# Kernel tuning notes

Measured on AMD Instinct MI355X. Metric: run time of the kernel, lower is better.

Reference implementation:

```python
import jax, jax.numpy as jnp
import numpy as np

EMBED_DIM = 512
NUM_JOINTS = 17
HIDDEN = EMBED_DIM * 2  # hidden_ratio=2
B, T = 32, 243


def setup_inputs() -> dict:
    key = jax.random.key(0)
    k_x, k_w1, k_w2 = jax.random.split(key, 3)
    x = jax.random.normal(k_x, (B, T, NUM_JOINTS, EMBED_DIM), dtype=jnp.float32)
    # kaiming_uniform with a=sqrt(5): bound = sqrt(6 / ((1 + a^2) * fan_in)) = sqrt(1/fan_in)
    b1 = float(np.sqrt(1.0 / EMBED_DIM))
    fc1_w = jax.random.uniform(k_w1, (NUM_JOINTS, EMBED_DIM, HIDDEN), minval=-b1, maxval=b1, dtype=jnp.float32)
    fc1_b = jnp.zeros((NUM_JOINTS, HIDDEN), dtype=jnp.float32)
    b2 = float(np.sqrt(1.0 / HIDDEN))
    fc2_w = jax.random.uniform(k_w2, (NUM_JOINTS, HIDDEN, 3), minval=-b2, maxval=b2, dtype=jnp.float32)
    fc2_b = jnp.zeros((NUM_JOINTS, 3), dtype=jnp.float32)
    ln_gamma = jnp.ones((EMBED_DIM,), dtype=jnp.float32)
    ln_beta = jnp.zeros((EMBED_DIM,), dtype=jnp.float32)
    return {"x": x, "ln_gamma": ln_gamma, "ln_beta": ln_beta,
            "fc1_w": fc1_w, "fc1_b": fc1_b, "fc2_w": fc2_w, "fc2_b": fc2_b}


def _layernorm(x, gamma, beta, eps=1e-5):
    mu = jnp.mean(x, axis=-1, keepdims=True)
    var = jnp.mean(jnp.square(x - mu), axis=-1, keepdims=True)
    return (x - mu) * jax.lax.rsqrt(var + eps) * gamma + beta


def reference(x, ln_gamma, ln_beta, fc1_w, fc1_b, fc2_w, fc2_b):
    # x: [B, T, J, d] -> [B, T, J, 3]
    xn = _layernorm(x, ln_gamma, ln_beta)
    h = jnp.einsum('btjd,jdh->btjh', xn, fc1_w) + fc1_b  # [B,T,J,H]
    h = jax.nn.gelu(h, approximate=False)  # torch GELU default is exact (erf)
    y = jnp.einsum('btjh,jho->btjo', h, fc2_w) + fc2_b  # [B,T,J,3]
    return y
```

## Files before the change

kernel.cpp:

```cpp
#include <hip/hip_runtime.h>
#include <hip/hip_bf16.h>

#define JN   17
#define DIM  512
#define HID  1024
#define MTOT 7776
#define MPAD 7808
#define BN   256
#define NTHR 512

typedef __attribute__((ext_vector_type(8))) short s16x8;
typedef __attribute__((ext_vector_type(4))) float f32x4;
typedef unsigned short ushort_t;

__device__ __forceinline__ unsigned int f2bf(float f) {
    return (unsigned int)__builtin_bit_cast(unsigned short, __float2bfloat16(f));
}

__device__ __forceinline__ float gelu_erf(float h) {
    float ah = fabsf(h);
    float z  = ah * 0.7071067811865476f;
    float t  = __builtin_amdgcn_rcpf(fmaf(0.3275911f, z, 1.0f));
    float p  = fmaf(fmaf(fmaf(fmaf(1.061405429f, t, -1.453152027f), t,
                              1.421413741f), t, -0.284496736f), t, 0.254829592f);
    float er = 1.0f - p * t * __expf(-z * z);
    return fmaf(0.5f * ah, er, 0.5f * h);
}

__global__ __launch_bounds__(256)
void prep_w1(const float* __restrict__ w1, ushort_t* __restrict__ w1s) {
    int b  = blockIdx.x;
    int nq = b & 3;
    int kc = (b >> 2) & 15;
    int j  = b >> 6;
    int n  = nq * 256 + threadIdx.x;

    const float* src = w1 + ((size_t)j * DIM + kc * 32) * HID + n;
    ushort_t* dst = w1s + (((size_t)j * 16 + kc) * 1024 + n) * 32;

    #pragma unroll
    for (int u = 0; u < 4; ++u) {
        float v[8];
        #pragma unroll
        for (int e = 0; e < 8; ++e) v[e] = src[(u * 8 + e) * HID];
        uint4 qq;
        qq.x = f2bf(v[0]) | (f2bf(v[1]) << 16);
        qq.y = f2bf(v[2]) | (f2bf(v[3]) << 16);
        qq.z = f2bf(v[4]) | (f2bf(v[5]) << 16);
        qq.w = f2bf(v[6]) | (f2bf(v[7]) << 16);
        int p = u ^ ((n >> 1) & 3);
        *(uint4*)(dst + p * 8) = qq;
    }
}

__global__ __launch_bounds__(NTHR)
void prep_xn(const float* __restrict__ x,
             const float* __restrict__ gamma,
             const float* __restrict__ beta,
             ushort_t* __restrict__ xa)
{
    const int lane = threadIdx.x & 63;
    const int wv   = threadIdx.x >> 6;
    const int m    = blockIdx.x * 8 + wv;
    const int j    = blockIdx.y;

    const float4* gp = (const float4*)(gamma + lane * 8);
    const float4* bp = (const float4*)(beta + lane * 8);
    float4 g0 = gp[0], g1 = gp[1];
    float4 e0 = bp[0], e1 = bp[1];

    const float4* xp = (const float4*)(x + ((size_t)m * JN + j) * DIM + lane * 8);
    float4 va = xp[0], vb = xp[1];

    float s  = ((va.x + va.y) + (va.z + va.w)) + ((vb.x + vb.y) + (vb.z + vb.w));
    float s2 = fmaf(va.x, va.x, fmaf(va.y, va.y, fmaf(va.z, va.z, fmaf(va.w, va.w,
               fmaf(vb.x, vb.x, fmaf(vb.y, vb.y, fmaf(vb.z, vb.z, vb.w * vb.w)))))));
    #pragma unroll
    for (int d = 1; d < 64; d <<= 1) {
        s  += __shfl_xor(s,  d);
        s2 += __shfl_xor(s2, d);
    }
    float mu  = s * (1.0f / 512.0f);
    float var = s2 * (1.0f / 512.0f) - mu * mu;
    float rs  = rsqrtf(var + 1e-5f);

    float v0 = fmaf((va.x - mu) * rs, g0.x, e0.x);
    float v1 = fmaf((va.y - mu) * rs, g0.y, e0.y);
    float v2 = fmaf((va.z - mu) * rs, g0.z, e0.z);
    float v3 = fmaf((va.w - mu) * rs, g0.w, e0.w);
    float v4 = fmaf((vb.x - mu) * rs, g1.x, e1.x);
    float v5 = fmaf((vb.y - mu) * rs, g1.y, e1.y);
    float v6 = fmaf((vb.z - mu) * rs, g1.z, e1.z);
    float v7 = fmaf((vb.w - mu) * rs, g1.w, e1.w);
    uint4 qq;
    qq.x = f2bf(v0) | (f2bf(v1) << 16);
    qq.y = f2bf(v2) | (f2bf(v3) << 16);
    qq.z = f2bf(v4) | (f2bf(v5) << 16);
    qq.w = f2bf(v6) | (f2bf(v7) << 16);

    int kc = lane >> 2;
    int p  = (lane & 3) ^ (m & 3) ^ ((m >> 2) & 3);
    *(uint4*)(xa + (((size_t)j * 16 + kc) * MPAD + m) * 32 + p * 8) = qq;
}

#define SLOT6   24576
#define SMEM_V8 49152
#define NWG    (61 * 4 * JN)

__global__ __launch_bounds__(NTHR, 4)
void pjh_gemm_v8(const ushort_t* __restrict__ xa,
                 const ushort_t* __restrict__ w1s,
                 const float* __restrict__ b1,
                 const float* __restrict__ w2,
                 float* __restrict__ ypart)
{
    extern __shared__ char smem[];
    const int tid  = threadIdx.x;
    const int lane = tid & 63;
    const int wv   = tid >> 6;
    const int wm   = wv >> 2;
    const int wn   = wv & 3;

    const int q   = NWG / 8, r = NWG % 8;
    const int xcd = blockIdx.x & 7;
    const int lid = blockIdx.x >> 3;
    const int work = ((xcd < r) ? xcd * (q + 1) : r * (q + 1) + (xcd - r) * q) + lid;
    const int nt = work & 3;
    const int wrest = work >> 2;
    const int mt = wrest % 61;
    const int j  = wrest / 61;

    const ushort_t* aSrc = xa  + (size_t)j * 16 * MPAD * 32
                               + (size_t)mt * 128 * 32 + tid * 8;
    const ushort_t* bSrc = w1s + (size_t)j * 16 * 1024 * 32
                               + (size_t)nt * 256 * 32 + (size_t)(wv * 2) * 512 + lane * 8;

    int aoffs[4], boffs[4];
    {
        const int g = lane >> 4;
        #pragma unroll
        for (int mf = 0; mf < 4; ++mf) {
            int ml = wm * 64 + mf * 16 + (lane & 15);
            int p  = g ^ (ml & 3) ^ ((ml >> 2) & 3);
            aoffs[mf] = ml * 64 + p * 16;
        }
        #pragma unroll
        for (int nf = 0; nf < 4; ++nf) {
            int nl = wn * 64 + nf * 16 + (lane & 15);
            int p  = g ^ ((nl >> 1) & 3);
            boffs[nf] = 8192 + (nl * 4 + p) * 16;
        }
    }

#define ISSUE8(SBASE) do {                                                     \
        __builtin_amdgcn_global_load_lds(                                      \
            (const __attribute__((address_space(1))) unsigned int*)aSrc,       \
            (__attribute__((address_space(3))) unsigned int*)(smem + (SBASE) + wv * 1024), \
            16, 0, 0);                                                         \
        __builtin_amdgcn_global_load_lds(                                      \
            (const __attribute__((address_space(1))) unsigned int*)bSrc,       \
            (__attribute__((address_space(3))) unsigned int*)(smem + (SBASE) + 8192 + wv * 2048), \
            16, 0, 0);                                                         \
        __builtin_amdgcn_global_load_lds(                                      \
            (const __attribute__((address_space(1))) unsigned int*)(bSrc + 512), \
            (__attribute__((address_space(3))) unsigned int*)(smem + (SBASE) + 8192 + wv * 2048 + 1024), \
            16, 0, 0);                                                         \
        aSrc += (size_t)MPAD * 32;                                             \
        bSrc += 32768;                                                         \
    } while (0)

#define STEP8(SBASE) do {                                                      \
        s16x8 aF[4], bF[4];                                                    \
        _Pragma("unroll")                                                      \
        for (int mf = 0; mf < 4; ++mf)                                         \
            aF[mf] = *(const s16x8*)(smem + (SBASE) + aoffs[mf]);              \
        _Pragma("unroll")                                                      \
        for (int nf = 0; nf < 4; ++nf)                                         \
            bF[nf] = *(const s16x8*)(smem + (SBASE) + boffs[nf]);              \
        __builtin_amdgcn_s_setprio(1);                                         \
        _Pragma("unroll")                                                      \
        for (int mf = 0; mf < 4; ++mf)                                         \
            _Pragma("unroll")                                                  \
            for (int nf = 0; nf < 4; ++nf)                                     \
                acc[mf][nf] = __builtin_amdgcn_mfma_f32_16x16x32_bf16(aF[mf], bF[nf], acc[mf][nf], 0, 0, 0); \
        __builtin_amdgcn_s_setprio(0);                                         \
    } while (0)

    const f32x4 zero4 = {0.f, 0.f, 0.f, 0.f};
    f32x4 acc[4][4];
    #pragma unroll
    for (int mf = 0; mf < 4; ++mf)
        #pragma unroll
        for (int nf = 0; nf < 4; ++nf) acc[mf][nf] = zero4;

    ISSUE8(0);
    __syncthreads();

    #pragma unroll 1
    for (int tp = 0; tp < 8; ++tp) {
        ISSUE8(SLOT6);
        STEP8(0);
        __syncthreads();
        if (tp < 7) {
            ISSUE8(0);
        }
        STEP8(SLOT6);
        __syncthreads();
    }

    float yr[4][4][3];
    #pragma unroll
    for (int a = 0; a < 4; ++a)
        #pragma unroll
        for (int rr = 0; rr < 4; ++rr)
            #pragma unroll
            for (int o = 0; o < 3; ++o) yr[a][rr][o] = 0.f;

    #pragma unroll
    for (int nf = 0; nf < 4; ++nf) {
        int n = nt * BN + wn * 64 + nf * 16 + (lane & 15);
        float b1v = b1[j * HID + n];
        const float* w2p = w2 + ((size_t)j * HID + n) * 3;
        float w20 = w2p[0], w21 = w2p[1], w22 = w2p[2];
        #pragma unroll
        for (int mf = 0; mf < 4; ++mf) {
            #pragma unroll
            for (int rr = 0; rr < 4; ++rr) {
                float gv = gelu_erf(acc[mf][nf][rr] + b1v);
                yr[mf][rr][0] = fmaf(gv, w20, yr[mf][rr][0]);
                yr[mf][rr][1] = fmaf(gv, w21, yr[mf][rr][1]);
                yr[mf][rr][2] = fmaf(gv, w22, yr[mf][rr][2]);
            }
        }
    }

    #pragma unroll
    for (int mf = 0; mf < 4; ++mf)
        #pragma unroll
        for (int rr = 0; rr < 4; ++rr)
            #pragma unroll
            for (int o = 0; o < 3; ++o) {
                float v = yr[mf][rr][o];
                v += __shfl_xor(v, 1);
                v += __shfl_xor(v, 2);
                v += __shfl_xor(v, 4);
                v += __shfl_xor(v, 8);
                yr[mf][rr][o] = v;
            }

    float* Yp = (float*)smem;
    if ((lane & 15) == 0) {
        int mrow = lane >> 4;
        #pragma unroll
        for (int mf = 0; mf < 4; ++mf)
            #pragma unroll
            for (int rr = 0; rr < 4; ++rr) {
                int m = wm * 64 + mf * 16 + mrow * 4 + rr;
                #pragma unroll
                for (int o = 0; o < 3; ++o)
                    Yp[(wn * 128 + m) * 3 + o] = yr[mf][rr][o];
            }
    }
    __syncthreads();

    if (tid < 128 * 3) {
        int m = tid / 3;
        int o = tid - m * 3;
        int gr = mt * 128 + m;
        float v = Yp[m * 3 + o] + Yp[(128 + m) * 3 + o]
                + Yp[(2 * 128 + m) * 3 + o] + Yp[(3 * 128 + m) * 3 + o];
        ypart[(((size_t)nt * MPAD + gr) * JN + j) * 3 + o] = v;
    }
#undef ISSUE8
#undef STEP8
}

__global__ __launch_bounds__(512)
void fc2_reduce(const float* __restrict__ ypart,
                const float* __restrict__ b2,
                float* __restrict__ out)
{
    int idx = blockIdx.x * 512 + threadIdx.x;
    if (idx >= MTOT * JN * 3) return;
    int rest = idx / 3;
    int o = idx - rest * 3;
    int j = rest % JN;
    float v = b2[j * 3 + o]
            + ypart[idx]
            + ypart[(size_t)MPAD * JN * 3 + idx]
            + ypart[(size_t)2 * MPAD * JN * 3 + idx]
            + ypart[(size_t)3 * MPAD * JN * 3 + idx];
    out[idx] = v;
}

#define BM3 96
#define A3_OFF 0
#define B3_OFF 98304
#define Y3_OFF 98304
#define SMEM_V3 163840

__global__ __launch_bounds__(NTHR, 2)
void pjh_fused_v3(const float* __restrict__ x,
                  const float* __restrict__ gamma,
                  const float* __restrict__ beta,
                  const ushort_t* __restrict__ w1s,
                  const float* __restrict__ b1,
                  const float* __restrict__ w2,
                  const float* __restrict__ b2,
                  float* __restrict__ out)
{
    extern __shared__ char smem[];
    const int tid  = threadIdx.x;
    const int lane = tid & 63;
    const int wv   = tid >> 6;
    const int wm   = wv >> 2;
    const int wn   = wv & 3;
    const int mt   = blockIdx.x;
    const int j    = blockIdx.y;

    const ushort_t* w1j = w1s + (size_t)j * 16 * 1024 * 32;

    #pragma unroll
    for (int tt = 0; tt < 2; ++tt) {
        const ushort_t* tb = w1j + (size_t)tt * 1024 * 32;
        #pragma unroll
        for (int qq = 0; qq < 2; ++qq) {
            const ushort_t* src = tb + (size_t)(wv * 2 + qq) * 512 + lane * 8;
            void* dst = smem + B3_OFF + tt * 16384 + (wv * 2 + qq) * 1024;
            __builtin_amdgcn_global_load_lds(
                (const __attribute__((address_space(1))) unsigned int*)src,
                (__attribute__((address_space(3))) unsigned int*)dst, 16, 0, 0);
        }
    }

    {
        const float4* gp  = (const float4*)(gamma + lane * 8);
        const float4* bpp = (const float4*)(beta + lane * 8);
        float4 g0 = gp[0], g1 = gp[1];
        float4 e0 = bpp[0], e1 = bpp[1];
        #pragma unroll
        for (int rb = 0; rb < 12; rb += 4) {
            float4 xs[4][2];
            #pragma unroll
            for (int rr = 0; rr < 4; ++rr) {
                int gr = mt * BM3 + wv * 12 + rb + rr;
                const float4* xp = (const float4*)(x + ((size_t)gr * JN + j) * DIM + lane * 8);
                xs[rr][0] = xp[0]; xs[rr][1] = xp[1];
            }
            #pragma unroll
            for (int rr = 0; rr < 4; ++rr) {
                int m = wv * 12 + rb + rr;
                float4 va = xs[rr][0], vb = xs[rr][1];
                float s  = ((va.x + va.y) + (va.z + va.w)) + ((vb.x + vb.y) + (vb.z + vb.w));
                float s2 = fmaf(va.x, va.x, fmaf(va.y, va.y, fmaf(va.z, va.z, fmaf(va.w, va.w,
                           fmaf(vb.x, vb.x, fmaf(vb.y, vb.y, fmaf(vb.z, vb.z, vb.w * vb.w)))))));
                #pragma unroll
                for (int d = 1; d < 64; d <<= 1) {
                    s  += __shfl_xor(s,  d);
                    s2 += __shfl_xor(s2, d);
                }
                float mu  = s * (1.0f / 512.0f);
                float var = s2 * (1.0f / 512.0f) - mu * mu;
                float rs  = rsqrtf(var + 1e-5f);
                float v0 = fmaf((va.x - mu) * rs, g0.x, e0.x);
                float v1 = fmaf((va.y - mu) * rs, g0.y, e0.y);
                float v2 = fmaf((va.z - mu) * rs, g0.z, e0.z);
                float v3 = fmaf((va.w - mu) * rs, g0.w, e0.w);
                float v4 = fmaf((vb.x - mu) * rs, g1.x, e1.x);
                float v5 = fmaf((vb.y - mu) * rs, g1.y, e1.y);
                float v6 = fmaf((vb.z - mu) * rs, g1.z, e1.z);
                float v7 = fmaf((vb.w - mu) * rs, g1.w, e1.w);
                uint4 qq;
                qq.x = f2bf(v0) | (f2bf(v1) << 16);
                qq.y = f2bf(v2) | (f2bf(v3) << 16);
                qq.z = f2bf(v4) | (f2bf(v5) << 16);
                qq.w = f2bf(v6) | (f2bf(v7) << 16);
                *(uint4*)(smem + A3_OFF + m * 1024 + ((lane ^ (m & 7)) * 16)) = qq;
            }
        }
    }

    __syncthreads();

    float yr[3][4][3];
    #pragma unroll
    for (int a = 0; a < 3; ++a)
        #pragma unroll
        for (int rr = 0; rr < 4; ++rr)
            #pragma unroll
            for (int o = 0; o < 3; ++o) yr[a][rr][o] = 0.f;

    const f32x4 zero4 = {0.f, 0.f, 0.f, 0.f};
    f32x4 acc[3][4];
    #pragma unroll
    for (int mf = 0; mf < 3; ++mf)
        #pragma unroll
        for (int nf = 0; nf < 4; ++nf) acc[mf][nf] = zero4;

    #pragma unroll 1
    for (int t = 0; t < 64; ++t) {
        if (t + 2 < 64) {
            int kc = (t + 2) & 15, nt = (t + 2) >> 4;
            const ushort_t* tb = w1j + ((size_t)kc * 1024 + nt * 256) * 32;
            int bb = ((t + 2) & 3) * 16384;
            #pragma unroll
            for (int qq = 0; qq < 2; ++qq) {
                const ushort_t* src = tb + (size_t)(wv * 2 + qq) * 512 + lane * 8;
                void* dst = smem + B3_OFF + bb + (wv * 2 + qq) * 1024;
                __builtin_amdgcn_global_load_lds(
                    (const __attribute__((address_space(1))) unsigned int*)src,
                    (__attribute__((address_space(3))) unsigned int*)dst, 16, 0, 0);
            }
        }

        int kc = t & 15;
        int bb = (t & 3) * 16384;
        int g  = lane >> 4;
        s16x8 aF[3], bF[4];
        #pragma unroll
        for (int mf = 0; mf < 3; ++mf) {
            int m  = wm * 48 + mf * 16 + (lane & 15);
            int ul = kc * 4 + g;
            aF[mf] = *(const s16x8*)(smem + A3_OFF + m * 1024 + ((ul ^ (m & 7)) * 16));
        }
        #pragma unroll
        for (int nf = 0; nf < 4; ++nf) {
            int nl = wn * 64 + nf * 16 + (lane & 15);
            int p  = g ^ ((nl >> 1) & 3);
            bF[nf] = *(const s16x8*)(smem + B3_OFF + bb + (nl * 4 + p) * 16);
        }

        __builtin_amdgcn_s_setprio(1);
        #pragma unroll
        for (int mf = 0; mf < 3; ++mf)
            #pragma unroll
            for (int nf = 0; nf < 4; ++nf)
                acc[mf][nf] = __builtin_amdgcn_mfma_f32_16x16x32_bf16(aF[mf], bF[nf], acc[mf][nf], 0, 0, 0);
        __builtin_amdgcn_s_setprio(0);

        if ((t & 15) == 15) {
            int nt = t >> 4;
            #pragma unroll
            for (int nf = 0; nf < 4; ++nf) {
                int n = nt * BN + wn * 64 + nf * 16 + (lane & 15);
                float b1v = b1[j * HID + n];
                const float* w2p = w2 + ((size_t)j * HID + n) * 3;
                float w20 = w2p[0], w21 = w2p[1], w22 = w2p[2];
                #pragma unroll
                for (int mf = 0; mf < 3; ++mf) {
                    #pragma unroll
                    for (int rr = 0; rr < 4; ++rr) {
                        float gv = gelu_erf(acc[mf][nf][rr] + b1v);
                        yr[mf][rr][0] = fmaf(gv, w20, yr[mf][rr][0]);
                        yr[mf][rr][1] = fmaf(gv, w21, yr[mf][rr][1]);
                        yr[mf][rr][2] = fmaf(gv, w22, yr[mf][rr][2]);
                    }
                }
            }
            #pragma unroll
            for (int mf = 0; mf < 3; ++mf)
                #pragma unroll
                for (int nf = 0; nf < 4; ++nf)
                    acc[mf][nf] = zero4;
        }

        if (t < 62) {
            asm volatile("s_waitcnt vmcnt(2)" ::: "memory");
        } else {
            asm volatile("s_waitcnt vmcnt(0)" ::: "memory");
        }
        __builtin_amdgcn_s_barrier();
    }

    #pragma unroll
    for (int mf = 0; mf < 3; ++mf)
        #pragma unroll
        for (int rr = 0; rr < 4; ++rr)
            #pragma unroll
            for (int o = 0; o < 3; ++o) {
                float v = yr[mf][rr][o];
                v += __shfl_xor(v, 1);
                v += __shfl_xor(v, 2);
                v += __shfl_xor(v, 4);
                v += __shfl_xor(v, 8);
                yr[mf][rr][o] = v;
            }

    __syncthreads();

    float* Yp = (float*)(smem + Y3_OFF);
    if ((lane & 15) == 0) {
        int mrow = lane >> 4;
        #pragma unroll
        for (int mf = 0; mf < 3; ++mf)
            #pragma unroll
            for (int rr = 0; rr < 4; ++rr) {
                int m = wm * 48 + mf * 16 + mrow * 4 + rr;
                #pragma unroll
                for (int o = 0; o < 3; ++o)
                    Yp[(wn * BM3 + m) * 3 + o] = yr[mf][rr][o];
            }
    }
    __syncthreads();

    if (tid < BM3 * 3) {
        int m = tid / 3;
        int o = tid - m * 3;
        int gr = mt * BM3 + m;
        float v = Yp[m * 3 + o] + Yp[(BM3 + m) * 3 + o]
                + Yp[(2 * BM3 + m) * 3 + o] + Yp[(3 * BM3 + m) * 3 + o]
                + b2[j * 3 + o];
        out[((size_t)gr * JN + j) * 3 + o] = v;
    }
}

extern "C" void kernel_launch(void* const* d_in, const int* in_sizes, int n_in,
                              void* d_out, int out_size, void* d_ws, size_t ws_size,
                              hipStream_t stream) {
    (void)in_sizes; (void)n_in; (void)out_size;
    const float* x   = (const float*)d_in[0];
    const float* ga  = (const float*)d_in[1];
    const float* be  = (const float*)d_in[2];
    const float* w1  = (const float*)d_in[3];
    const float* b1  = (const float*)d_in[4];
    const float* w2  = (const float*)d_in[5];
    const float* b2  = (const float*)d_in[6];
    float* out = (float*)d_out;

    const size_t xa_bytes  = (size_t)JN * 16 * MPAD * 32 * sizeof(ushort_t);
    const size_t w1s_bytes = (size_t)JN * 16 * 1024 * 32 * sizeof(ushort_t);
    const size_t yp_bytes  = (size_t)4 * MPAD * JN * 3 * sizeof(float);

    if (ws_size >= xa_bytes + w1s_bytes + yp_bytes) {
        ushort_t* xa  = (ushort_t*)d_ws;
        ushort_t* w1s = (ushort_t*)((char*)d_ws + xa_bytes);
        float* ypart  = (float*)((char*)d_ws + xa_bytes + w1s_bytes);
        prep_xn<<<dim3(MTOT / 8, JN), NTHR, 0, stream>>>(x, ga, be, xa);
        prep_w1<<<JN * 16 * 4, 256, 0, stream>>>(w1, w1s);
        hipFuncSetAttribute((const void*)pjh_gemm_v8,
                            hipFuncAttributeMaxDynamicSharedMemorySize, SMEM_V8);
        pjh_gemm_v8<<<NWG, NTHR, SMEM_V8, stream>>>(xa, w1s, b1, w2, ypart);
        fc2_reduce<<<(MTOT * JN * 3 + 511) / 512, 512, 0, stream>>>(ypart, b2, out);
    } else {
        ushort_t* w1s = (ushort_t*)d_ws;
        prep_w1<<<JN * 16 * 4, 256, 0, stream>>>(w1, w1s);
        hipFuncSetAttribute((const void*)pjh_fused_v3,
                            hipFuncAttributeMaxDynamicSharedMemorySize, SMEM_V3);
        dim3 grid(MTOT / BM3, JN);
        pjh_fused_v3<<<grid, NTHR, SMEM_V3, stream>>>(x, ga, be, w1s, b1, w2, b2, out);
    }
}
```

Measured before the change: 315.7 us.

## Load MFMA fragments directly from global into registers, dropping LDS staging

The GEMM kernel no longer stages A and B tiles through LDS with global_load_lds and barriers. Each wave now loads its bf16 fragments straight from global memory into a double-buffered register set. The tile shrinks to 128x128 with 256 threads, so the N dimension splits into 8 partial outputs and the reduction kernel sums 8 slices. The xa layout drops its swizzle to match the direct loads. This removes LDS traffic and synchronisation, at the cost of redundant global/L2 reads across waves, higher register pressure and a larger partial-sum buffer.

```diff
diff --git a/kernel.cpp b/kernel.cpp
--- a/kernel.cpp
+++ b/kernel.cpp
@@ -6,7 +6,6 @@
 #define HID  1024
 #define MTOT 7776
 #define MPAD 7808
-#define BN   256
 #define NTHR 512
 
 typedef __attribute__((ext_vector_type(8))) short s16x8;
@@ -99,90 +98,56 @@
     qq.w = f2bf(v6) | (f2bf(v7) << 16);
 
     int kc = lane >> 2;
-    int p  = (lane & 3) ^ (m & 3) ^ ((m >> 2) & 3);
-    *(uint4*)(xa + (((size_t)j * 16 + kc) * MPAD + m) * 32 + p * 8) = qq;
-}
-
-#define SLOT6   24576
-#define SMEM_V8 49152
-#define NWG    (61 * 4 * JN)
-
-__global__ __launch_bounds__(NTHR, 4)
-void pjh_gemm_v8(const ushort_t* __restrict__ xa,
+    *(uint4*)(xa + (((size_t)j * 16 + kc) * MPAD + m) * 32 + (lane & 3) * 8) = qq;
+}
+
+#define NWG9 (61 * 8 * JN)
+
+__global__ __launch_bounds__(256, 3)
+void pjh_gemm_v9(const ushort_t* __restrict__ xa,
                  const ushort_t* __restrict__ w1s,
                  const float* __restrict__ b1,
                  const float* __restrict__ w2,
                  float* __restrict__ ypart)
 {
-    extern __shared__ char smem[];
+    __shared__ float Yp[2 * 128 * 3];
     const int tid  = threadIdx.x;
     const int lane = tid & 63;
     const int wv   = tid >> 6;
-    const int wm   = wv >> 2;
-    const int wn   = wv & 3;
-
-    const int q   = NWG / 8, r = NWG % 8;
-    const int xcd = blockIdx.x & 7;
-    const int lid = blockIdx.x >> 3;
-    const int work = ((xcd < r) ? xcd * (q + 1) : r * (q + 1) + (xcd - r) * q) + lid;
-    const int nt = work & 3;
-    const int wrest = work >> 2;
-    const int mt = wrest % 61;
-    const int j  = wrest / 61;
-
-    const ushort_t* aSrc = xa  + (size_t)j * 16 * MPAD * 32
-                               + (size_t)mt * 128 * 32 + tid * 8;
-    const ushort_t* bSrc = w1s + (size_t)j * 16 * 1024 * 32
-                               + (size_t)nt * 256 * 32 + (size_t)(wv * 2) * 512 + lane * 8;
-
-    int aoffs[4], boffs[4];
-    {
-        const int g = lane >> 4;
-        #pragma unroll
-        for (int mf = 0; mf < 4; ++mf) {
-            int ml = wm * 64 + mf * 16 + (lane & 15);
-            int p  = g ^ (ml & 3) ^ ((ml >> 2) & 3);
-            aoffs[mf] = ml * 64 + p * 16;
-        }
-        #pragma unroll
-        for (int nf = 0; nf < 4; ++nf) {
-            int nl = wn * 64 + nf * 16 + (lane & 15);
-            int p  = g ^ ((nl >> 1) & 3);
-            boffs[nf] = 8192 + (nl * 4 + p) * 16;
-        }
-    }
-
-#define ISSUE8(SBASE) do {                                                     \
-        __builtin_amdgcn_global_load_lds(                                      \
-            (const __attribute__((address_space(1))) unsigned int*)aSrc,       \
-            (__attribute__((address_space(3))) unsigned int*)(smem + (SBASE) + wv * 1024), \
-            16, 0, 0);                                                         \
-        __builtin_amdgcn_global_load_lds(                                      \
-            (const __attribute__((address_space(1))) unsigned int*)bSrc,       \
-            (__attribute__((address_space(3))) unsigned int*)(smem + (SBASE) + 8192 + wv * 2048), \
-            16, 0, 0);                                                         \
-        __builtin_amdgcn_global_load_lds(                                      \
-            (const __attribute__((address_space(1))) unsigned int*)(bSrc + 512), \
-            (__attribute__((address_space(3))) unsigned int*)(smem + (SBASE) + 8192 + wv * 2048 + 1024), \
-            16, 0, 0);                                                         \
-        aSrc += (size_t)MPAD * 32;                                             \
-        bSrc += 32768;                                                         \
+    const int wm   = wv >> 1;
+    const int wn   = wv & 1;
+
+    const int xcd  = blockIdx.x & 7;
+    const int lid  = blockIdx.x >> 3;
+    const int work = xcd * (NWG9 / 8) + lid;
+    const int nt2  = work & 7;
+    const int wrest = work >> 3;
+    const int mt   = wrest % 61;
+    const int j    = wrest / 61;
+
+    const int g = lane >> 4;
+    const ushort_t* aB = xa + (size_t)j * 16 * MPAD * 32
+                            + ((size_t)mt * 128 + wm * 64 + (lane & 15)) * 32 + g * 8;
+    const int pB = g ^ (((lane & 15) >> 1) & 3);
+    const ushort_t* bB = w1s + (size_t)j * 16 * 1024 * 32
+                             + ((size_t)nt2 * 128 + wn * 64 + (lane & 15)) * 32 + pB * 8;
+
+#define LOADSET(FA, FB) do {                                                   \
+        _Pragma("unroll")                                                      \
+        for (int mf = 0; mf < 4; ++mf) FA[mf] = *(const s16x8*)(aB + mf * 512);\
+        _Pragma("unroll")                                                      \
+        for (int nf = 0; nf < 4; ++nf) FB[nf] = *(const s16x8*)(bB + nf * 512);\
+        aB += (size_t)MPAD * 32;                                               \
+        bB += 32768;                                                           \
     } while (0)
 
-#define STEP8(SBASE) do {                                                      \
-        s16x8 aF[4], bF[4];                                                    \
-        _Pragma("unroll")                                                      \
-        for (int mf = 0; mf < 4; ++mf)                                         \
-            aF[mf] = *(const s16x8*)(smem + (SBASE) + aoffs[mf]);              \
-        _Pragma("unroll")                                                      \
-        for (int nf = 0; nf < 4; ++nf)                                         \
-            bF[nf] = *(const s16x8*)(smem + (SBASE) + boffs[nf]);              \
+#define COMPUTE(FA, FB) do {                                                   \
         __builtin_amdgcn_s_setprio(1);                                         \
         _Pragma("unroll")                                                      \
         for (int mf = 0; mf < 4; ++mf)                                         \
             _Pragma("unroll")                                                  \
             for (int nf = 0; nf < 4; ++nf)                                     \
-                acc[mf][nf] = __builtin_amdgcn_mfma_f32_16x16x32_bf16(aF[mf], bF[nf], acc[mf][nf], 0, 0, 0); \
+                acc[mf][nf] = __builtin_amdgcn_mfma_f32_16x16x32_bf16(FA[mf], FB[nf], acc[mf][nf], 0, 0, 0); \
         __builtin_amdgcn_s_setprio(0);                                         \
     } while (0)
 
@@ -193,20 +158,19 @@
         #pragma unroll
         for (int nf = 0; nf < 4; ++nf) acc[mf][nf] = zero4;
 
-    ISSUE8(0);
-    __syncthreads();
-
+    s16x8 fA0[4], fB0[4], fA1[4], fB1[4];
+
+    LOADSET(fA0, fB0);
+    LOADSET(fA1, fB1);
     #pragma unroll 1
-    for (int tp = 0; tp < 8; ++tp) {
-        ISSUE8(SLOT6);
-        STEP8(0);
-        __syncthreads();
-        if (tp < 7) {
-            ISSUE8(0);
-        }
-        STEP8(SLOT6);
-        __syncthreads();
-    }
+    for (int tp = 0; tp < 7; ++tp) {
+        COMPUTE(fA0, fB0);
+        LOADSET(fA0, fB0);
+        COMPUTE(fA1, fB1);
+        LOADSET(fA1, fB1);
+    }
+    COMPUTE(fA0, fB0);
+    COMPUTE(fA1, fB1);
 
     float yr[4][4][3];
     #pragma unroll
@@ -218,7 +182,7 @@
 
     #pragma unroll
     for (int nf = 0; nf < 4; ++nf) {
-        int n = nt * BN + wn * 64 + nf * 16 + (lane & 15);
+        int n = nt2 * 128 + wn * 64 + nf * 16 + (lane & 15);
         float b1v = b1[j * HID + n];
         const float* w2p = w2 + ((size_t)j * HID + n) * 3;
         float w20 = w2p[0], w21 = w2p[1], w22 = w2p[2];
@@ -248,7 +212,6 @@
                 yr[mf][rr][o] = v;
             }
 
-    float* Yp = (float*)smem;
     if ((lane & 15) == 0) {
         int mrow = lane >> 4;
         #pragma unroll
@@ -263,16 +226,17 @@
     }
     __syncthreads();
 
-    if (tid < 128 * 3) {
-        int m = tid / 3;
-        int o = tid - m * 3;
+    for (int idx = tid; idx < 128 * 3; idx += 256) {
+        int m = idx / 3;
+        int o = idx - m * 3;
         int gr = mt * 128 + m;
-        float v = Yp[m * 3 + o] + Yp[(128 + m) * 3 + o]
-                + Yp[(2 * 128 + m) * 3 + o] + Yp[(3 * 128 + m) * 3 + o];
-        ypart[(((size_t)nt * MPAD + gr) * JN + j) * 3 + o] = v;
-    }
-#undef ISSUE8
-#undef STEP8
+        if (gr < MTOT) {
+            float v = Yp[m * 3 + o] + Yp[(128 + m) * 3 + o];
+            ypart[(((size_t)nt2 * MPAD + gr) * JN + j) * 3 + o] = v;
+        }
+    }
+#undef LOADSET
+#undef COMPUTE
 }
 
 __global__ __launch_bounds__(512)
@@ -285,11 +249,10 @@
     int rest = idx / 3;
     int o = idx - rest * 3;
     int j = rest % JN;
-    float v = b2[j * 3 + o]
-            + ypart[idx]
-            + ypart[(size_t)MPAD * JN * 3 + idx]
-            + ypart[(size_t)2 * MPAD * JN * 3 + idx]
-            + ypart[(size_t)3 * MPAD * JN * 3 + idx];
+    const size_t sl = (size_t)MPAD * JN * 3;
+    float v = b2[j * 3 + o];
+    #pragma unroll
+    for (int s = 0; s < 8; ++s) v += ypart[s * sl + idx];
     out[idx] = v;
 }
 
@@ -442,7 +405,7 @@
             int nt = t >> 4;
             #pragma unroll
             for (int nf = 0; nf < 4; ++nf) {
-                int n = nt * BN + wn * 64 + nf * 16 + (lane & 15);
+                int n = nt * 256 + wn * 64 + nf * 16 + (lane & 15);
                 float b1v = b1[j * HID + n];
                 const float* w2p = w2 + ((size_t)j * HID + n) * 3;
                 float w20 = w2p[0], w21 = w2p[1], w22 = w2p[2];
@@ -529,7 +492,7 @@
 
     const size_t xa_bytes  = (size_t)JN * 16 * MPAD * 32 * sizeof(ushort_t);
     const size_t w1s_bytes = (size_t)JN * 16 * 1024 * 32 * sizeof(ushort_t);
-    const size_t yp_bytes  = (size_t)4 * MPAD * JN * 3 * sizeof(float);
+    const size_t yp_bytes  = (size_t)8 * MPAD * JN * 3 * sizeof(float);
 
     if (ws_size >= xa_bytes + w1s_bytes + yp_bytes) {
         ushort_t* xa  = (ushort_t*)d_ws;
@@ -537,9 +500,7 @@
         float* ypart  = (float*)((char*)d_ws + xa_bytes + w1s_bytes);
         prep_xn<<<dim3(MTOT / 8, JN), NTHR, 0, stream>>>(x, ga, be, xa);
         prep_w1<<<JN * 16 * 4, 256, 0, stream>>>(w1, w1s);
-        hipFuncSetAttribute((const void*)pjh_gemm_v8,
-                            hipFuncAttributeMaxDynamicSharedMemorySize, SMEM_V8);
-        pjh_gemm_v8<<<NWG, NTHR, SMEM_V8, stream>>>(xa, w1s, b1, w2, ypart);
+        pjh_gemm_v9<<<NWG9, 256, 0, stream>>>(xa, w1s, b1, w2, ypart);
         fc2_reduce<<<(MTOT * JN * 3 + 511) / 512, 512, 0, stream>>>(ypart, b2, out);
     } else {
         ushort_t* w1s = (ushort_t*)d_ws;
```

New measurement: 330.9 us. 1.05x slower.
